# Optimization experiments

Hardware: AMD Instinct MI355X
Metric: run time of the kernel (lower is better)

The kernel has to match this reference:

```python
import jax, jax.numpy as jnp
import numpy as np

DIM = 2048


def setup_inputs() -> dict:
    key = jax.random.key(0)
    ks = jax.random.split(key, 9)
    scale = 1.0 / np.sqrt(DIM)
    x = jax.random.normal(ks[0], (4, 4096, DIM), dtype=jnp.float32)
    def lin(kw, kb):
        W = jax.random.uniform(kw, (DIM, DIM), jnp.float32, -scale, scale)
        b = jax.random.uniform(kb, (DIM,), jnp.float32, -scale, scale)
        return W, b
    Wq, bq = lin(ks[1], ks[2])
    Wk, bk = lin(ks[3], ks[4])
    Wv, bv = lin(ks[5], ks[6])
    Wg, bg = lin(ks[7], ks[8])
    return {"x": x, "Wq": Wq, "bq": bq, "Wk": Wk, "bk": bk,
            "Wv": Wv, "bv": bv, "Wg": Wg, "bg": bg}


def reference(x, Wq, bq, Wk, bk, Wv, bv, Wg, bg):
    # torch nn.Linear: y = x @ W.T + b
    q = jnp.einsum('bsd,ed->bse', x, Wq) + bq
    k = jnp.einsum('bsd,ed->bse', x, Wk) + bk
    v = jnp.einsum('bsd,ed->bse', x, Wv) + bv
    g = jax.nn.sigmoid(jnp.einsum('bsd,ed->bse', x, Wg) + bg)
    kv_state = jnp.cumsum(k * v, axis=1)  # O(N) associative state along seq
    return q * kv_state * g
```

## Files before the change

### kernel.cpp

```cpp
#include <hip/hip_runtime.h>
#include <stdint.h>

#define DIM   2048
#define BATCH 4
#define SEQ   4096
#define NTOK  (BATCH*SEQ)
#define NCH   128
#define CHUNK (SEQ/NCH)

#define XB_BYTES   ((size_t)NTOK*DIM*2)
#define WB_BYTES   ((size_t)4*DIM*DIM*2)
#define Y_BYTES    ((size_t)4*NTOK*DIM*2)
#define PART_BYTES ((size_t)BATCH*NCH*DIM*4)

typedef __bf16 bf16x8 __attribute__((ext_vector_type(8)));
typedef float  f32x4  __attribute__((ext_vector_type(4)));

__device__ __forceinline__ unsigned short f2bf(float f) {
  unsigned int u = __float_as_uint(f);
  u += 0x7FFFu + ((u >> 16) & 1u);
  return (unsigned short)(u >> 16);
}
__device__ __forceinline__ float bflo(unsigned int u){ return __uint_as_float(u << 16); }
__device__ __forceinline__ float bfhi(unsigned int u){ return __uint_as_float(u & 0xFFFF0000u); }
__device__ __forceinline__ float sigm(float x){ return 1.0f/(1.0f + __expf(-x)); }

__device__ __forceinline__ void gload16(const void* g, void* l) {
  __builtin_amdgcn_global_load_lds((const __attribute__((address_space(1))) unsigned int*)g,
                                   (__attribute__((address_space(3))) unsigned int*)l,
                                   16, 0, 0);
}

__global__ void cvt_kernel(const float* __restrict__ src,
                           unsigned short* __restrict__ dst, int n8) {
  int i = blockIdx.x * blockDim.x + threadIdx.x;
  if (i >= n8) return;
  const float4* s4 = (const float4*)src;
  float4 a = s4[2*i], b = s4[2*i+1];
  uint4 o;
  o.x = (unsigned int)f2bf(a.x) | ((unsigned int)f2bf(a.y) << 16);
  o.y = (unsigned int)f2bf(a.z) | ((unsigned int)f2bf(a.w) << 16);
  o.z = (unsigned int)f2bf(b.x) | ((unsigned int)f2bf(b.y) << 16);
  o.w = (unsigned int)f2bf(b.z) | ((unsigned int)f2bf(b.w) << 16);
  ((uint4*)dst)[i] = o;
}

__global__ void cvt_w_kernel(const float* __restrict__ Wq, const float* __restrict__ Wk,
                             const float* __restrict__ Wv, const float* __restrict__ Wg,
                             unsigned short* __restrict__ dst) {
  const int z = blockIdx.y;
  const float* src = (z == 0) ? Wq : (z == 1) ? Wk : (z == 2) ? Wv : Wg;
  int i = blockIdx.x * blockDim.x + threadIdx.x;
  const float4* s4 = (const float4*)src;
  float4 a = s4[2*i], b = s4[2*i+1];
  uint4 o;
  o.x = (unsigned int)f2bf(a.x) | ((unsigned int)f2bf(a.y) << 16);
  o.y = (unsigned int)f2bf(a.z) | ((unsigned int)f2bf(a.w) << 16);
  o.z = (unsigned int)f2bf(b.x) | ((unsigned int)f2bf(b.y) << 16);
  o.w = (unsigned int)f2bf(b.z) | ((unsigned int)f2bf(b.w) << 16);
  ((uint4*)(dst + (size_t)z * DIM * DIM))[i] = o;
}

__global__ __launch_bounds__(256, 2)
void gemm_kernel(const unsigned short* __restrict__ xb,
                 const unsigned short* __restrict__ Wall,
                 const float* __restrict__ bq, const float* __restrict__ bk,
                 const float* __restrict__ bv, const float* __restrict__ bg,
                 unsigned short* __restrict__ Yall) {
  __shared__ __align__(16) unsigned short ldsA[128*32];
  __shared__ __align__(16) unsigned short ldsB[128*32];

  const int t  = threadIdx.x;
  const int e0 = blockIdx.x * 128;
  const int m0 = blockIdx.y * 128;
  const int z  = blockIdx.z;
  const unsigned short* Wz = Wall + (size_t)z * DIM * DIM;

  const int r0 = t >> 2;
  const int cc = (t & 3) ^ (r0 & 3);
  const unsigned short* gA0 = xb + (size_t)(m0 + r0) * DIM + cc * 8;
  const unsigned short* gA1 = gA0 + (size_t)64 * DIM;
  const unsigned short* gB0 = Wz + (size_t)(e0 + r0) * DIM + cc * 8;
  const unsigned short* gB1 = gB0 + (size_t)64 * DIM;
  unsigned short* lA0 = &ldsA[(size_t)t * 8];
  unsigned short* lA1 = &ldsA[(size_t)(t + 256) * 8];
  unsigned short* lB0 = &ldsB[(size_t)t * 8];
  unsigned short* lB1 = &ldsB[(size_t)(t + 256) * 8];

  const int lane = t & 63;
  const int wave = t >> 6;
  const int wm = wave >> 1, wn = wave & 1;
  const int lr = lane & 15, lq = lane >> 4;
  const int swz8 = (lq ^ (lr & 3)) * 8;
  int aoff[4], boff[4];
  #pragma unroll
  for (int i = 0; i < 4; i++) aoff[i] = (wm*64 + i*16 + lr)*32 + swz8;
  #pragma unroll
  for (int j = 0; j < 4; j++) boff[j] = (wn*64 + j*16 + lr)*32 + swz8;

  f32x4 acc[4][4];
  #pragma unroll
  for (int i = 0; i < 4; i++)
    #pragma unroll
    for (int j = 0; j < 4; j++)
      acc[i][j] = (f32x4){0.f, 0.f, 0.f, 0.f};

  for (int kt = 0; kt < DIM/32; ++kt) {
    __syncthreads();
    const int ko = kt * 32;
    gload16(gA0 + ko, lA0);
    gload16(gA1 + ko, lA1);
    gload16(gB0 + ko, lB0);
    gload16(gB1 + ko, lB1);
    __syncthreads();

    bf16x8 a[4], b[4];
    #pragma unroll
    for (int i = 0; i < 4; i++) a[i] = *(const bf16x8*)&ldsA[aoff[i]];
    #pragma unroll
    for (int j = 0; j < 4; j++) b[j] = *(const bf16x8*)&ldsB[boff[j]];
    #pragma unroll
    for (int i = 0; i < 4; i++)
      #pragma unroll
      for (int j = 0; j < 4; j++)
        acc[i][j] = __builtin_amdgcn_mfma_f32_16x16x32_bf16(a[i], b[j], acc[i][j], 0, 0, 0);
  }

  const float* bias = (z == 0) ? bq : (z == 1) ? bk : (z == 2) ? bv : bg;
  unsigned short* Y = Yall + (size_t)z * NTOK * DIM;
  #pragma unroll
  for (int j = 0; j < 4; j++) {
    const int e = e0 + wn*64 + j*16 + lr;
    const float bb = bias[e];
    #pragma unroll
    for (int i = 0; i < 4; i++) {
      const int mb = m0 + wm*64 + i*16 + lq*4;
      #pragma unroll
      for (int r = 0; r < 4; r++)
        Y[(size_t)(mb + r) * DIM + e] = f2bf(acc[i][j][r] + bb);
    }
  }
}

__global__ void chunk_sum_kernel(const unsigned short* __restrict__ Yk,
                                 const unsigned short* __restrict__ Yv,
                                 float* __restrict__ partial) {
  const int d8 = threadIdx.x;
  const int c = blockIdx.y, b = blockIdx.z;
  const size_t base = (size_t)(b*SEQ + c*CHUNK) * (DIM/8) + d8;
  const uint4* pk = (const uint4*)Yk + base;
  const uint4* pv = (const uint4*)Yv + base;
  float s[8] = {0.f,0.f,0.f,0.f,0.f,0.f,0.f,0.f};
  #pragma unroll 4
  for (int i = 0; i < CHUNK; i++) {
    uint4 ku = pk[(size_t)i*(DIM/8)];
    uint4 vu = pv[(size_t)i*(DIM/8)];
    s[0] += bflo(ku.x)*bflo(vu.x);  s[1] += bfhi(ku.x)*bfhi(vu.x);
    s[2] += bflo(ku.y)*bflo(vu.y);  s[3] += bfhi(ku.y)*bfhi(vu.y);
    s[4] += bflo(ku.z)*bflo(vu.z);  s[5] += bfhi(ku.z)*bfhi(vu.z);
    s[6] += bflo(ku.w)*bflo(vu.w);  s[7] += bfhi(ku.w)*bfhi(vu.w);
  }
  float4* pp = (float4*)(partial + (size_t)(b*NCH + c)*DIM + d8*8);
  pp[0] = make_float4(s[0], s[1], s[2], s[3]);
  pp[1] = make_float4(s[4], s[5], s[6], s[7]);
}

__global__ void scan_kernel(float* __restrict__ partial) {
  const int idx = blockIdx.x * blockDim.x + threadIdx.x;
  const int b = idx >> 11;
  const int d = idx & (DIM - 1);
  float run = 0.f;
  for (int c = 0; c < NCH; c++) {
    float* p = partial + (size_t)(b*NCH + c)*DIM + d;
    float tv = *p;
    *p = run;
    run += tv;
  }
}

__global__ void final_kernel(const unsigned short* __restrict__ Yq,
                             const unsigned short* __restrict__ Yk,
                             const unsigned short* __restrict__ Yv,
                             const unsigned short* __restrict__ Yg,
                             const float* __restrict__ partial,
                             float* __restrict__ out) {
  const int d8 = threadIdx.x;
  const int c = blockIdx.y, b = blockIdx.z;
  const size_t base = (size_t)(b*SEQ + c*CHUNK) * (DIM/8) + d8;
  const float4* pst = (const float4*)(partial + (size_t)(b*NCH + c)*DIM + d8*8);
  float4 st0 = pst[0], st1 = pst[1];
  float s[8] = {st0.x, st0.y, st0.z, st0.w, st1.x, st1.y, st1.z, st1.w};
  const uint4* pq = (const uint4*)Yq + base;
  const uint4* pk = (const uint4*)Yk + base;
  const uint4* pv = (const uint4*)Yv + base;
  const uint4* pg = (const uint4*)Yg + base;
  float4* po = (float4*)out + base*2;
  #pragma unroll 2
  for (int i = 0; i < CHUNK; i++) {
    uint4 ku = pk[(size_t)i*(DIM/8)];
    uint4 vu = pv[(size_t)i*(DIM/8)];
    uint4 qu = pq[(size_t)i*(DIM/8)];
    uint4 gu = pg[(size_t)i*(DIM/8)];
    s[0] += bflo(ku.x)*bflo(vu.x);  s[1] += bfhi(ku.x)*bfhi(vu.x);
    s[2] += bflo(ku.y)*bflo(vu.y);  s[3] += bfhi(ku.y)*bfhi(vu.y);
    s[4] += bflo(ku.z)*bflo(vu.z);  s[5] += bfhi(ku.z)*bfhi(vu.z);
    s[6] += bflo(ku.w)*bflo(vu.w);  s[7] += bfhi(ku.w)*bfhi(vu.w);
    float4 o0, o1;
    o0.x = bflo(qu.x)*s[0]*sigm(bflo(gu.x));  o0.y = bfhi(qu.x)*s[1]*sigm(bfhi(gu.x));
    o0.z = bflo(qu.y)*s[2]*sigm(bflo(gu.y));  o0.w = bfhi(qu.y)*s[3]*sigm(bfhi(gu.y));
    o1.x = bflo(qu.z)*s[4]*sigm(bflo(gu.z));  o1.y = bfhi(qu.z)*s[5]*sigm(bfhi(gu.z));
    o1.z = bflo(qu.w)*s[6]*sigm(bflo(gu.w));  o1.w = bfhi(qu.w)*s[7]*sigm(bfhi(gu.w));
    po[(size_t)i*(DIM/4)]     = o0;
    po[(size_t)i*(DIM/4) + 1] = o1;
  }
}

extern "C" void kernel_launch(void* const* d_in, const int* in_sizes, int n_in,
                              void* d_out, int out_size, void* d_ws, size_t ws_size,
                              hipStream_t stream) {
  const float* x  = (const float*)d_in[0];
  const float* Wq = (const float*)d_in[1];
  const float* bq = (const float*)d_in[2];
  const float* Wk = (const float*)d_in[3];
  const float* bk = (const float*)d_in[4];
  const float* Wv = (const float*)d_in[5];
  const float* bv = (const float*)d_in[6];
  const float* Wg = (const float*)d_in[7];
  const float* bg = (const float*)d_in[8];
  float* out = (float*)d_out;

  char* ws = (char*)d_ws;
  unsigned short* xb      = (unsigned short*)(ws);
  unsigned short* Wall    = (unsigned short*)(ws + XB_BYTES);
  unsigned short* Yall    = (unsigned short*)(ws + XB_BYTES + WB_BYTES);
  float*          partial = (float*)(ws + XB_BYTES + WB_BYTES + Y_BYTES);

  {
    int n8 = NTOK * DIM / 8;
    cvt_kernel<<<n8 / 256, 256, 0, stream>>>(x, xb, n8);
    int w8 = DIM * DIM / 8;
    cvt_w_kernel<<<dim3(w8 / 256, 4), 256, 0, stream>>>(Wq, Wk, Wv, Wg, Wall);
  }

  gemm_kernel<<<dim3(DIM/128, NTOK/128, 4), 256, 0, stream>>>(
      xb, Wall, bq, bk, bv, bg, Yall);

  const unsigned short* Yq = Yall + 0*(size_t)NTOK*DIM;
  const unsigned short* Yk = Yall + 1*(size_t)NTOK*DIM;
  const unsigned short* Yv = Yall + 2*(size_t)NTOK*DIM;
  const unsigned short* Yg = Yall + 3*(size_t)NTOK*DIM;

  chunk_sum_kernel<<<dim3(1, NCH, BATCH), 256, 0, stream>>>(Yk, Yv, partial);
  scan_kernel<<<(BATCH*DIM)/256, 256, 0, stream>>>(partial);
  final_kernel<<<dim3(1, NCH, BATCH), 256, 0, stream>>>(Yq, Yk, Yv, Yg, partial, out);
}
```

Before: 999.4 us.

## Fuse projection pairs in GEMM epilogue and parallelize chunk-prefix scan

```diff
diff --git a/kernel.cpp b/kernel.cpp
--- a/kernel.cpp
+++ b/kernel.cpp
@@ -5,12 +5,12 @@
 #define BATCH 4
 #define SEQ   4096
 #define NTOK  (BATCH*SEQ)
-#define NCH   128
+#define NCH   256
 #define CHUNK (SEQ/NCH)
 
 #define XB_BYTES   ((size_t)NTOK*DIM*2)
 #define WB_BYTES   ((size_t)4*DIM*DIM*2)
-#define Y_BYTES    ((size_t)4*NTOK*DIM*2)
+#define PW_BYTES   ((size_t)2*NTOK*DIM*2)
 #define PART_BYTES ((size_t)BATCH*NCH*DIM*4)
 
 typedef __bf16 bf16x8 __attribute__((ext_vector_type(8)));
@@ -66,26 +66,33 @@
                  const unsigned short* __restrict__ Wall,
                  const float* __restrict__ bq, const float* __restrict__ bk,
                  const float* __restrict__ bv, const float* __restrict__ bg,
-                 unsigned short* __restrict__ Yall) {
-  __shared__ __align__(16) unsigned short ldsA[128*32];
-  __shared__ __align__(16) unsigned short ldsB[128*32];
+                 unsigned short* __restrict__ Yw,
+                 unsigned short* __restrict__ Yp) {
+  __shared__ __align__(16) unsigned short ldsA [128*32];
+  __shared__ __align__(16) unsigned short ldsBa[128*32];
+  __shared__ __align__(16) unsigned short ldsBb[128*32];
 
   const int t  = threadIdx.x;
   const int e0 = blockIdx.x * 128;
   const int m0 = blockIdx.y * 128;
-  const int z  = blockIdx.z;
-  const unsigned short* Wz = Wall + (size_t)z * DIM * DIM;
+  const int zg = blockIdx.z;
+  const unsigned short* Wa = Wall + (size_t)(zg == 0 ? 0 : 1) * DIM * DIM;
+  const unsigned short* Wb = Wall + (size_t)(zg == 0 ? 3 : 2) * DIM * DIM;
 
   const int r0 = t >> 2;
   const int cc = (t & 3) ^ (r0 & 3);
   const unsigned short* gA0 = xb + (size_t)(m0 + r0) * DIM + cc * 8;
   const unsigned short* gA1 = gA0 + (size_t)64 * DIM;
-  const unsigned short* gB0 = Wz + (size_t)(e0 + r0) * DIM + cc * 8;
-  const unsigned short* gB1 = gB0 + (size_t)64 * DIM;
-  unsigned short* lA0 = &ldsA[(size_t)t * 8];
-  unsigned short* lA1 = &ldsA[(size_t)(t + 256) * 8];
-  unsigned short* lB0 = &ldsB[(size_t)t * 8];
-  unsigned short* lB1 = &ldsB[(size_t)(t + 256) * 8];
+  const unsigned short* gBa0 = Wa + (size_t)(e0 + r0) * DIM + cc * 8;
+  const unsigned short* gBa1 = gBa0 + (size_t)64 * DIM;
+  const unsigned short* gBb0 = Wb + (size_t)(e0 + r0) * DIM + cc * 8;
+  const unsigned short* gBb1 = gBb0 + (size_t)64 * DIM;
+  unsigned short* lA0  = &ldsA [(size_t)t * 8];
+  unsigned short* lA1  = &ldsA [(size_t)(t + 256) * 8];
+  unsigned short* lBa0 = &ldsBa[(size_t)t * 8];
+  unsigned short* lBa1 = &ldsBa[(size_t)(t + 256) * 8];
+  unsigned short* lBb0 = &ldsBb[(size_t)t * 8];
+  unsigned short* lBb1 = &ldsBb[(size_t)(t + 256) * 8];
 
   const int lane = t & 63;
   const int wave = t >> 6;
@@ -98,90 +105,119 @@
   #pragma unroll
   for (int j = 0; j < 4; j++) boff[j] = (wn*64 + j*16 + lr)*32 + swz8;
 
-  f32x4 acc[4][4];
+  f32x4 accA[4][4], accB[4][4];
   #pragma unroll
   for (int i = 0; i < 4; i++)
     #pragma unroll
-    for (int j = 0; j < 4; j++)
-      acc[i][j] = (f32x4){0.f, 0.f, 0.f, 0.f};
+    for (int j = 0; j < 4; j++) {
+      accA[i][j] = (f32x4){0.f, 0.f, 0.f, 0.f};
+      accB[i][j] = (f32x4){0.f, 0.f, 0.f, 0.f};
+    }
 
   for (int kt = 0; kt < DIM/32; ++kt) {
     __syncthreads();
     const int ko = kt * 32;
-    gload16(gA0 + ko, lA0);
-    gload16(gA1 + ko, lA1);
-    gload16(gB0 + ko, lB0);
-    gload16(gB1 + ko, lB1);
+    gload16(gA0  + ko, lA0);
+    gload16(gA1  + ko, lA1);
+    gload16(gBa0 + ko, lBa0);
+    gload16(gBa1 + ko, lBa1);
+    gload16(gBb0 + ko, lBb0);
+    gload16(gBb1 + ko, lBb1);
     __syncthreads();
 
-    bf16x8 a[4], b[4];
+    bf16x8 a[4];
     #pragma unroll
     for (int i = 0; i < 4; i++) a[i] = *(const bf16x8*)&ldsA[aoff[i]];
-    #pragma unroll
-    for (int j = 0; j < 4; j++) b[j] = *(const bf16x8*)&ldsB[boff[j]];
-    #pragma unroll
-    for (int i = 0; i < 4; i++)
-      #pragma unroll
-      for (int j = 0; j < 4; j++)
-        acc[i][j] = __builtin_amdgcn_mfma_f32_16x16x32_bf16(a[i], b[j], acc[i][j], 0, 0, 0);
-  }
-
-  const float* bias = (z == 0) ? bq : (z == 1) ? bk : (z == 2) ? bv : bg;
-  unsigned short* Y = Yall + (size_t)z * NTOK * DIM;
+    {
+      bf16x8 b[4];
+      #pragma unroll
+      for (int j = 0; j < 4; j++) b[j] = *(const bf16x8*)&ldsBa[boff[j]];
+      #pragma unroll
+      for (int i = 0; i < 4; i++)
+        #pragma unroll
+        for (int j = 0; j < 4; j++)
+          accA[i][j] = __builtin_amdgcn_mfma_f32_16x16x32_bf16(a[i], b[j], accA[i][j], 0, 0, 0);
+    }
+    {
+      bf16x8 b[4];
+      #pragma unroll
+      for (int j = 0; j < 4; j++) b[j] = *(const bf16x8*)&ldsBb[boff[j]];
+      #pragma unroll
+      for (int i = 0; i < 4; i++)
+        #pragma unroll
+        for (int j = 0; j < 4; j++)
+          accB[i][j] = __builtin_amdgcn_mfma_f32_16x16x32_bf16(a[i], b[j], accB[i][j], 0, 0, 0);
+    }
+  }
+
+  const float* biasA = (zg == 0) ? bq : bk;
+  const float* biasB = (zg == 0) ? bg : bv;
+  unsigned short* Y = (zg == 0) ? Yw : Yp;
   #pragma unroll
   for (int j = 0; j < 4; j++) {
     const int e = e0 + wn*64 + j*16 + lr;
-    const float bb = bias[e];
+    const float bA = biasA[e];
+    const float bB = biasB[e];
     #pragma unroll
     for (int i = 0; i < 4; i++) {
       const int mb = m0 + wm*64 + i*16 + lq*4;
       #pragma unroll
-      for (int r = 0; r < 4; r++)
-        Y[(size_t)(mb + r) * DIM + e] = f2bf(acc[i][j][r] + bb);
-    }
-  }
-}
-
-__global__ void chunk_sum_kernel(const unsigned short* __restrict__ Yk,
-                                 const unsigned short* __restrict__ Yv,
+      for (int r = 0; r < 4; r++) {
+        const float vA = accA[i][j][r] + bA;
+        const float vB = accB[i][j][r] + bB;
+        const float val = (zg == 0) ? (vA * sigm(vB)) : (vA * vB);
+        Y[(size_t)(mb + r) * DIM + e] = f2bf(val);
+      }
+    }
+  }
+}
+
+__global__ void chunk_sum_kernel(const unsigned short* __restrict__ Yp,
                                  float* __restrict__ partial) {
   const int d8 = threadIdx.x;
   const int c = blockIdx.y, b = blockIdx.z;
   const size_t base = (size_t)(b*SEQ + c*CHUNK) * (DIM/8) + d8;
-  const uint4* pk = (const uint4*)Yk + base;
-  const uint4* pv = (const uint4*)Yv + base;
+  const uint4* pp = (const uint4*)Yp + base;
   float s[8] = {0.f,0.f,0.f,0.f,0.f,0.f,0.f,0.f};
   #pragma unroll 4
   for (int i = 0; i < CHUNK; i++) {
-    uint4 ku = pk[(size_t)i*(DIM/8)];
-    uint4 vu = pv[(size_t)i*(DIM/8)];
-    s[0] += bflo(ku.x)*bflo(vu.x);  s[1] += bfhi(ku.x)*bfhi(vu.x);
-    s[2] += bflo(ku.y)*bflo(vu.y);  s[3] += bfhi(ku.y)*bfhi(vu.y);
-    s[4] += bflo(ku.z)*bflo(vu.z);  s[5] += bfhi(ku.z)*bfhi(vu.z);
-    s[6] += bflo(ku.w)*bflo(vu.w);  s[7] += bfhi(ku.w)*bfhi(vu.w);
-  }
-  float4* pp = (float4*)(partial + (size_t)(b*NCH + c)*DIM + d8*8);
-  pp[0] = make_float4(s[0], s[1], s[2], s[3]);
-  pp[1] = make_float4(s[4], s[5], s[6], s[7]);
+    uint4 pu = pp[(size_t)i*(DIM/8)];
+    s[0] += bflo(pu.x);  s[1] += bfhi(pu.x);
+    s[2] += bflo(pu.y);  s[3] += bfhi(pu.y);
+    s[4] += bflo(pu.z);  s[5] += bfhi(pu.z);
+    s[6] += bflo(pu.w);  s[7] += bfhi(pu.w);
+  }
+  float4* po = (float4*)(partial + (size_t)(b*NCH + c)*DIM + d8*8);
+  po[0] = make_float4(s[0], s[1], s[2], s[3]);
+  po[1] = make_float4(s[4], s[5], s[6], s[7]);
 }
 
 __global__ void scan_kernel(float* __restrict__ partial) {
-  const int idx = blockIdx.x * blockDim.x + threadIdx.x;
-  const int b = idx >> 11;
-  const int d = idx & (DIM - 1);
-  float run = 0.f;
-  for (int c = 0; c < NCH; c++) {
-    float* p = partial + (size_t)(b*NCH + c)*DIM + d;
-    float tv = *p;
-    *p = run;
-    run += tv;
-  }
-}
-
-__global__ void final_kernel(const unsigned short* __restrict__ Yq,
-                             const unsigned short* __restrict__ Yk,
-                             const unsigned short* __restrict__ Yv,
-                             const unsigned short* __restrict__ Yg,
+  const int wid  = (blockIdx.x * blockDim.x + threadIdx.x) >> 6;
+  const int lane = threadIdx.x & 63;
+  const int b = wid >> 11;
+  const int d = wid & (DIM - 1);
+  float* base = partial + (size_t)b * NCH * DIM + d;
+  float v[4];
+  #pragma unroll
+  for (int k = 0; k < 4; k++) v[k] = base[(size_t)(lane*4 + k) * DIM];
+  float sum = v[0] + v[1] + v[2] + v[3];
+  float inc = sum;
+  #pragma unroll
+  for (int off = 1; off < 64; off <<= 1) {
+    float n = __shfl_up(inc, off, 64);
+    if (lane >= off) inc += n;
+  }
+  float run = inc - sum;
+  #pragma unroll
+  for (int k = 0; k < 4; k++) {
+    base[(size_t)(lane*4 + k) * DIM] = run;
+    run += v[k];
+  }
+}
+
+__global__ void final_kernel(const unsigned short* __restrict__ Yw,
+                             const unsigned short* __restrict__ Yp,
                              const float* __restrict__ partial,
                              float* __restrict__ out) {
   const int d8 = threadIdx.x;
@@ -190,26 +226,22 @@
   const float4* pst = (const float4*)(partial + (size_t)(b*NCH + c)*DIM + d8*8);
   float4 st0 = pst[0], st1 = pst[1];
   float s[8] = {st0.x, st0.y, st0.z, st0.w, st1.x, st1.y, st1.z, st1.w};
-  const uint4* pq = (const uint4*)Yq + base;
-  const uint4* pk = (const uint4*)Yk + base;
-  const uint4* pv = (const uint4*)Yv + base;
-  const uint4* pg = (const uint4*)Yg + base;
+  const uint4* pw = (const uint4*)Yw + base;
+  const uint4* pp = (const uint4*)Yp + base;
   float4* po = (float4*)out + base*2;
   #pragma unroll 2
   for (int i = 0; i < CHUNK; i++) {
-    uint4 ku = pk[(size_t)i*(DIM/8)];
-    uint4 vu = pv[(size_t)i*(DIM/8)];
-    uint4 qu = pq[(size_t)i*(DIM/8)];
-    uint4 gu = pg[(size_t)i*(DIM/8)];
-    s[0] += bflo(ku.x)*bflo(vu.x);  s[1] += bfhi(ku.x)*bfhi(vu.x);
-    s[2] += bflo(ku.y)*bflo(vu.y);  s[3] += bfhi(ku.y)*bfhi(vu.y);
-    s[4] += bflo(ku.z)*bflo(vu.z);  s[5] += bfhi(ku.z)*bfhi(vu.z);
-    s[6] += bflo(ku.w)*bflo(vu.w);  s[7] += bfhi(ku.w)*bfhi(vu.w);
+    uint4 pu = pp[(size_t)i*(DIM/8)];
+    uint4 wu = pw[(size_t)i*(DIM/8)];
+    s[0] += bflo(pu.x);  s[1] += bfhi(pu.x);
+    s[2] += bflo(pu.y);  s[3] += bfhi(pu.y);
+    s[4] += bflo(pu.z);  s[5] += bfhi(pu.z);
+    s[6] += bflo(pu.w);  s[7] += bfhi(pu.w);
     float4 o0, o1;
-    o0.x = bflo(qu.x)*s[0]*sigm(bflo(gu.x));  o0.y = bfhi(qu.x)*s[1]*sigm(bfhi(gu.x));
-    o0.z = bflo(qu.y)*s[2]*sigm(bflo(gu.y));  o0.w = bfhi(qu.y)*s[3]*sigm(bfhi(gu.y));
-    o1.x = bflo(qu.z)*s[4]*sigm(bflo(gu.z));  o1.y = bfhi(qu.z)*s[5]*sigm(bfhi(gu.z));
-    o1.z = bflo(qu.w)*s[6]*sigm(bflo(gu.w));  o1.w = bfhi(qu.w)*s[7]*sigm(bfhi(gu.w));
+    o0.x = bflo(wu.x)*s[0];  o0.y = bfhi(wu.x)*s[1];
+    o0.z = bflo(wu.y)*s[2];  o0.w = bfhi(wu.y)*s[3];
+    o1.x = bflo(wu.z)*s[4];  o1.y = bfhi(wu.z)*s[5];
+    o1.z = bflo(wu.w)*s[6];  o1.w = bfhi(wu.w)*s[7];
     po[(size_t)i*(DIM/4)]     = o0;
     po[(size_t)i*(DIM/4) + 1] = o1;
   }
@@ -232,8 +264,9 @@
   char* ws = (char*)d_ws;
   unsigned short* xb      = (unsigned short*)(ws);
   unsigned short* Wall    = (unsigned short*)(ws + XB_BYTES);
-  unsigned short* Yall    = (unsigned short*)(ws + XB_BYTES + WB_BYTES);
-  float*          partial = (float*)(ws + XB_BYTES + WB_BYTES + Y_BYTES);
+  unsigned short* Yw      = (unsigned short*)(ws + XB_BYTES + WB_BYTES);
+  unsigned short* Yp      = Yw + (size_t)NTOK * DIM;
+  float*          partial = (float*)(ws + XB_BYTES + WB_BYTES + PW_BYTES);
 
   {
     int n8 = NTOK * DIM / 8;
@@ -242,15 +275,10 @@
     cvt_w_kernel<<<dim3(w8 / 256, 4), 256, 0, stream>>>(Wq, Wk, Wv, Wg, Wall);
   }
 
-  gemm_kernel<<<dim3(DIM/128, NTOK/128, 4), 256, 0, stream>>>(
-      xb, Wall, bq, bk, bv, bg, Yall);
-
-  const unsigned short* Yq = Yall + 0*(size_t)NTOK*DIM;
-  const unsigned short* Yk = Yall + 1*(size_t)NTOK*DIM;
-  const unsigned short* Yv = Yall + 2*(size_t)NTOK*DIM;
-  const unsigned short* Yg = Yall + 3*(size_t)NTOK*DIM;
-
-  chunk_sum_kernel<<<dim3(1, NCH, BATCH), 256, 0, stream>>>(Yk, Yv, partial);
-  scan_kernel<<<(BATCH*DIM)/256, 256, 0, stream>>>(partial);
-  final_kernel<<<dim3(1, NCH, BATCH), 256, 0, stream>>>(Yq, Yk, Yv, Yg, partial, out);
-}
+  gemm_kernel<<<dim3(DIM/128, NTOK/128, 2), 256, 0, stream>>>(
+      xb, Wall, bq, bk, bv, bg, Yw, Yp);
+
+  chunk_sum_kernel<<<dim3(1, NCH, BATCH), 256, 0, stream>>>(Yp, partial);
+  scan_kernel<<<(BATCH*DIM*64)/256, 256, 0, stream>>>(partial);
+  final_kernel<<<dim3(1, NCH, BATCH), 256, 0, stream>>>(Yw, Yp, partial, out);
+}
```

After: 895.5 us. 1.12x faster.
